# Optimization experiments

Measured on AMD Instinct MI355X. Metric: run time of the kernel, lower is better.

Reference implementation:

```python
import jax, jax.numpy as jnp
import numpy as np

B, C, N, K = 1, 64, 65536, 16

def setup_inputs() -> dict:
    key = jax.random.key(0)
    ks = jax.random.split(key, 12)
    s = 0.02
    return {
        "spa": jax.random.normal(ks[0], (B, C, N), jnp.float32),
        "spe": jax.random.normal(ks[1], (B, C, N), jnp.float32),
        "neighbor_indices": jax.random.randint(ks[2], (B, N, K), 0, N, jnp.int64),
        # spa_MHA params (torch Linear weights, shape [out,in])
        "WQ_spa": jax.random.normal(ks[3], (C, C), jnp.float32) * s,
        "WK_spa": jax.random.normal(ks[4], (C, C), jnp.float32) * s,
        "WV_spa": jax.random.normal(ks[5], (C, C), jnp.float32) * s,
        "bV_spa": jnp.zeros((C,), jnp.float32),
        # spe_MHA params
        "WQ_spe": jax.random.normal(ks[6], (C, C), jnp.float32) * s,
        "WK_spe": jax.random.normal(ks[7], (C, C), jnp.float32) * s,
        "WV_spe": jax.random.normal(ks[8], (C, C), jnp.float32) * s,
        "bV_spe": jnp.zeros((C,), jnp.float32),
    }


def _cross_att(q, nb, WQ, WK, WV, bV):
    # q: [B,N,C], nb: [B,N,K,C]
    Q = jnp.einsum('bnc,dc->bnd', q, WQ)            # [B,N,C]
    Kk = jnp.einsum('bnkc,dc->bnkd', nb, WK)        # [B,N,K,C]
    V = jnp.einsum('bnkc,dc->bnkd', nb, WV) + bV    # [B,N,K,C]
    scores = jnp.einsum('bnd,bnkd->bnk', Q, Kk) / np.sqrt(Q.shape[-1]).astype(Q.dtype)
    attn = jax.nn.softmax(scores, axis=-1)          # [B,N,K]
    ctx = jnp.einsum('bnk,bnkd->bnd', attn, V)      # [B,N,C]
    return ctx.transpose(0, 2, 1)                   # [B,C,N]


def reference(spa, spe, neighbor_indices,
              WQ_spa, WK_spa, WV_spa, bV_spa,
              WQ_spe, WK_spe, WV_spe, bV_spe):
    dims = spa.shape[1]
    feature = jnp.concatenate([spa, spe], axis=1)   # [B,2C,N]
    # gather neighbors: [B,2C,N,K]
    nb = jax.vmap(lambda f, idx: f[:, idx])(feature, neighbor_indices)
    feature_q = feature.transpose(0, 2, 1)          # [B,N,2C]
    nb = nb.transpose(0, 2, 3, 1)                   # [B,N,K,2C]
    spa_feat = _cross_att(feature_q[..., :dims], nb[..., dims:],
                          WQ_spa, WK_spa, WV_spa, bV_spa)
    spe_feat = _cross_att(feature_q[..., dims:], nb[..., :dims],
                          WQ_spe, WK_spe, WV_spe, bV_spe)
    fusion = jnp.concatenate([spa_feat, spe_feat], axis=1)  # [B,2C,N]
    return feature + fusion
```

## Files before the change

### kernel.cpp

```cpp
#include <hip/hip_runtime.h>

#define NPTS 65536

__device__ __forceinline__ float bf_lo(unsigned u) { return __uint_as_float(u << 16); }
__device__ __forceinline__ float bf_hi(unsigned u) { return __uint_as_float(u & 0xFFFF0000u); }
__device__ __forceinline__ unsigned short f2bf(float f) {
    unsigned u = __float_as_uint(f);
    return (unsigned short)((u + 0x7FFFu + ((u >> 16) & 1u)) >> 16);
}
__device__ __forceinline__ unsigned pktrunc(float a, float b) {
    return (__float_as_uint(a) >> 16) | (__float_as_uint(b) & 0xFFFF0000u);
}
__device__ __forceinline__ void unpack8(uint4 v, float* o) {
    o[0] = bf_lo(v.x); o[1] = bf_hi(v.x); o[2] = bf_lo(v.y); o[3] = bf_hi(v.y);
    o[4] = bf_lo(v.z); o[5] = bf_hi(v.z); o[6] = bf_lo(v.w); o[7] = bf_hi(v.w);
}
#if __has_builtin(__builtin_amdgcn_fdot2_f32_bf16)
typedef __bf16 bf16x2 __attribute__((ext_vector_type(2)));
__device__ __forceinline__ float dot2acc(unsigned a, unsigned b, float c) {
    return __builtin_amdgcn_fdot2_f32_bf16(__builtin_bit_cast(bf16x2, a),
                                           __builtin_bit_cast(bf16x2, b), c, false);
}
#else
__device__ __forceinline__ float dot2acc(unsigned a, unsigned b, float c) {
    return c + bf_lo(a) * bf_lo(b) + bf_hi(a) * bf_hi(b);
}
#endif
#if __has_builtin(__builtin_amdgcn_rcpf)
__device__ __forceinline__ float fastrcp(float x) { return __builtin_amdgcn_rcpf(x); }
#else
__device__ __forceinline__ float fastrcp(float x) { return 1.0f / x; }
#endif

typedef __attribute__((ext_vector_type(8))) short short8;
typedef __attribute__((ext_vector_type(4))) float f32x4;

__global__ __launch_bounds__(256) void k_matM(const float* __restrict__ WQa,
                                              const float* __restrict__ WKa,
                                              const float* __restrict__ WQe,
                                              const float* __restrict__ WKe,
                                              unsigned short* __restrict__ Mt) {
    __shared__ float WKs[4096];
    __shared__ float WQs[64][16];
    const int which = blockIdx.x >> 2;
    const int c0 = (blockIdx.x & 3) * 16;
    const float* WQ = which ? WQe : WQa;
    const float* WK = which ? WKe : WKa;
    const int t = threadIdx.x;
    #pragma unroll
    for (int i = 0; i < 16; ++i) WKs[t + i * 256] = WK[t + i * 256];
    #pragma unroll
    for (int i = 0; i < 4; ++i) {
        const int id = t + i * 256;
        WQs[id >> 4][id & 15] = WQ[(id >> 4) * 64 + c0 + (id & 15)];
    }
    __syncthreads();
    const int cc = t >> 4;
    const int eg = t & 15;
    float a0 = 0.f, a1 = 0.f, a2 = 0.f, a3 = 0.f;
    #pragma unroll
    for (int d = 0; d < 64; ++d) {
        const float wq = WQs[d][cc];
        const float4 wk = *reinterpret_cast<const float4*>(&WKs[d * 64 + eg * 4]);
        a0 += wq * wk.x; a1 += wq * wk.y; a2 += wq * wk.z; a3 += wq * wk.w;
    }
    const int c = c0 + cc;
    Mt[which * 4096 + (eg * 4 + 0) * 64 + c] = f2bf(a0);
    Mt[which * 4096 + (eg * 4 + 1) * 64 + c] = f2bf(a1);
    Mt[which * 4096 + (eg * 4 + 2) * 64 + c] = f2bf(a2);
    Mt[which * 4096 + (eg * 4 + 3) * 64 + c] = f2bf(a3);
}

__global__ __launch_bounds__(256) void k_prep(const float* __restrict__ spa,
                                              const float* __restrict__ spe,
                                              const unsigned short* __restrict__ Mt,
                                              unsigned short* __restrict__ featT,
                                              unsigned short* __restrict__ qeff) {
    __shared__ unsigned short tb[64][136];
    __shared__ unsigned short ml[2][64][72];
    const int n0 = blockIdx.x * 64;
    const int t = threadIdx.x;
    #pragma unroll
    for (int i = 0; i < 4; ++i) {
        const int id = t + i * 256;
        const int which = id >> 9;
        const int row = (id >> 3) & 63;
        const int q = id & 7;
        *reinterpret_cast<uint4*>(&ml[which][row][q * 8]) =
            *reinterpret_cast<const uint4*>(Mt + which * 4096 + row * 64 + q * 8);
    }
    {
        const int p = t & 63;
        const int c0 = t >> 6;
        #pragma unroll
        for (int i = 0; i < 32; ++i) {
            const int c = c0 + (i << 2);
            const float v = (c < 64) ? spa[c * NPTS + n0 + p]
                                     : spe[(c - 64) * NPTS + n0 + p];
            tb[p][c] = f2bf(v);
        }
    }
    __syncthreads();
    {
        const int pt = t >> 2;
        const int q = t & 3;
        const uint4* src = reinterpret_cast<const uint4*>(&tb[pt][q * 32]);
        uint4* dst = reinterpret_cast<uint4*>(featT + (size_t)(n0 + pt) * 128 + q * 32);
        dst[0] = src[0]; dst[1] = src[1]; dst[2] = src[2]; dst[3] = src[3];
    }
    const int w = t >> 6;
    const int l = t & 63;
    const int lrow = l & 15;
    const int lk8 = (l >> 4) * 8;
    short8 afr[2][2];
    #pragma unroll
    for (int half = 0; half < 2; ++half)
        #pragma unroll
        for (int kc = 0; kc < 2; ++kc)
            afr[half][kc] = __builtin_bit_cast(short8,
                *reinterpret_cast<const uint4*>(&tb[w * 16 + lrow][half * 64 + kc * 32 + lk8]));
    f32x4 acc[8];
    #pragma unroll
    for (int et = 0; et < 8; ++et) acc[et] = (f32x4){0.f, 0.f, 0.f, 0.f};
    #pragma unroll
    for (int et = 0; et < 8; ++et) {
        const int which = et >> 2;
        const int el = (et & 3) * 16 + lrow;
        #pragma unroll
        for (int kc = 0; kc < 2; ++kc) {
            const short8 bfr = __builtin_bit_cast(short8,
                *reinterpret_cast<const uint4*>(&ml[which][el][kc * 32 + lk8]));
            acc[et] = __builtin_amdgcn_mfma_f32_16x16x32_bf16(afr[which][kc], bfr, acc[et], 0, 0, 0);
        }
    }
    #pragma unroll
    for (int et = 0; et < 8; ++et) {
        #pragma unroll
        for (int r = 0; r < 4; ++r) {
            const int n = n0 + w * 16 + (l >> 4) * 4 + r;
            qeff[(size_t)n * 128 + et * 16 + lrow] = f2bf(acc[et][r]);
        }
    }
}

__global__ __launch_bounds__(256) void k_attn(const unsigned short* __restrict__ featT,
                                              const unsigned short* __restrict__ qeff,
                                              const int* __restrict__ idx,
                                              unsigned short* __restrict__ sTb) {
    __shared__ unsigned red[4][16][68];
    const int wave = threadIdx.x >> 6;
    const int lane = threadIdx.x & 63;
    const int n = blockIdx.x * 4 + wave;
    const int k = lane >> 2;
    const int c4 = lane & 3;

    const int j = idx[n * 16 + k];
    const uint4* fx = reinterpret_cast<const uint4*>(featT + (size_t)j * 128);
    const uint4 A0 = fx[2*c4],     A1 = fx[2*c4 + 1];
    const uint4 E0 = fx[8 + 2*c4], E1 = fx[8 + 2*c4 + 1];
    const uint4* qx = reinterpret_cast<const uint4*>(qeff + (size_t)n * 128);
    const uint4 QA0 = qx[2*c4],     QA1 = qx[2*c4 + 1];
    const uint4 QE0 = qx[8 + 2*c4], QE1 = qx[8 + 2*c4 + 1];

    float pa = 0.f, pe = 0.f;
    pa = dot2acc(QA0.x, E0.x, pa); pa = dot2acc(QA0.y, E0.y, pa);
    pa = dot2acc(QA0.z, E0.z, pa); pa = dot2acc(QA0.w, E0.w, pa);
    pa = dot2acc(QA1.x, E1.x, pa); pa = dot2acc(QA1.y, E1.y, pa);
    pa = dot2acc(QA1.z, E1.z, pa); pa = dot2acc(QA1.w, E1.w, pa);
    pe = dot2acc(QE0.x, A0.x, pe); pe = dot2acc(QE0.y, A0.y, pe);
    pe = dot2acc(QE0.z, A0.z, pe); pe = dot2acc(QE0.w, A0.w, pe);
    pe = dot2acc(QE1.x, A1.x, pe); pe = dot2acc(QE1.y, A1.y, pe);
    pe = dot2acc(QE1.z, A1.z, pe); pe = dot2acc(QE1.w, A1.w, pe);
    pa += __shfl_xor(pa, 1); pa += __shfl_xor(pa, 2);
    pe += __shfl_xor(pe, 1); pe += __shfl_xor(pe, 2);
    const float ea = __expf(pa * 0.125f);
    const float ee = __expf(pe * 0.125f);
    float da = ea, de = ee;
    #pragma unroll
    for (int m = 4; m < 64; m <<= 1) {
        da += __shfl_xor(da, m);
        de += __shfl_xor(de, m);
    }
    const float wA = ea * fastrcp(da);
    const float wB = ee * fastrcp(de);

    float xa[16], xe[16];
    unpack8(A0, xa); unpack8(A1, xa + 8);
    unpack8(E0, xe); unpack8(E1, xe + 8);

    unsigned pA[8], pB[8];
    #pragma unroll
    for (int i = 0; i < 8; ++i) {
        pA[i] = pktrunc(wA * xe[2*i], wA * xe[2*i + 1]);
        pB[i] = pktrunc(wB * xa[2*i], wB * xa[2*i + 1]);
    }
    {
        uint4* wa4 = reinterpret_cast<uint4*>(&red[wave][k][c4 * 8]);
        wa4[0] = make_uint4(pA[0], pA[1], pA[2], pA[3]);
        wa4[1] = make_uint4(pA[4], pA[5], pA[6], pA[7]);
        uint4* wb4 = reinterpret_cast<uint4*>(&red[wave][k][32 + c4 * 8]);
        wb4[0] = make_uint4(pB[0], pB[1], pB[2], pB[3]);
        wb4[1] = make_uint4(pB[4], pB[5], pB[6], pB[7]);
    }
    asm volatile("s_waitcnt lgkmcnt(0)" ::: "memory");
    float s0 = 0.f, s1 = 0.f;
    #pragma unroll
    for (int kk = 0; kk < 16; ++kk) {
        const unsigned v = red[wave][kk][lane];
        s0 += __uint_as_float(v << 16);
        s1 += __uint_as_float(v & 0xFFFF0000u);
    }
    reinterpret_cast<unsigned*>(sTb + (size_t)n * 128)[lane] =
        (unsigned)f2bf(s0) | ((unsigned)f2bf(s1) << 16);
}

__global__ __launch_bounds__(256, 4) void k_out(const unsigned short* __restrict__ sTb,
                                                const float* __restrict__ spa,
                                                const float* __restrict__ spe,
                                                const float* __restrict__ WVa,
                                                const float* __restrict__ bVa,
                                                const float* __restrict__ WVe,
                                                const float* __restrict__ bVe,
                                                float* __restrict__ out) {
    __shared__ char smem_raw[27136];
    unsigned short* stile = reinterpret_cast<unsigned short*>(smem_raw);
    unsigned short* wvl = reinterpret_cast<unsigned short*>(smem_raw + 8704);
    float* ctxT = reinterpret_cast<float*>(smem_raw);
    const int n0 = blockIdx.x * 32;
    const int t = threadIdx.x;
    #pragma unroll
    for (int i = 0; i < 2; ++i) {
        const int id = t + i * 256;
        const int pt = id >> 4;
        const int q = id & 15;
        *reinterpret_cast<uint4*>(stile + pt * 136 + q * 8) =
            *reinterpret_cast<const uint4*>(sTb + (size_t)(n0 + pt) * 128 + q * 8);
    }
    #pragma unroll
    for (int i = 0; i < 32; ++i) {
        const int id = t + (i << 8);
        const int which = id >> 12;
        const int d = (id >> 6) & 63;
        const int e = id & 63;
        wvl[which * 4608 + d * 72 + e] = f2bf((which ? WVe : WVa)[d * 64 + e]);
    }
    __syncthreads();
    const int w = t >> 6;
    const int l = t & 63;
    const int half = w >> 1;
    const int pg = w & 1;
    const int lrow = l & 15;
    const int lk8 = (l >> 4) * 8;
    short8 afr[2];
    #pragma unroll
    for (int kc = 0; kc < 2; ++kc)
        afr[kc] = __builtin_bit_cast(short8,
            *reinterpret_cast<const uint4*>(stile + (pg * 16 + lrow) * 136 + half * 64 + kc * 32 + lk8));
    const unsigned short* wt = wvl + half * 4608;
    const float* bV = half ? bVe : bVa;
    f32x4 acc[4];
    #pragma unroll
    for (int nt = 0; nt < 4; ++nt) {
        acc[nt] = (f32x4){0.f, 0.f, 0.f, 0.f};
        #pragma unroll
        for (int kc = 0; kc < 2; ++kc) {
            const short8 bfr = __builtin_bit_cast(short8,
                *reinterpret_cast<const uint4*>(wt + (nt * 16 + lrow) * 72 + kc * 32 + lk8));
            acc[nt] = __builtin_amdgcn_mfma_f32_16x16x32_bf16(afr[kc], bfr, acc[nt], 0, 0, 0);
        }
    }
    __syncthreads();
    #pragma unroll
    for (int nt = 0; nt < 4; ++nt) {
        const int d = nt * 16 + lrow;
        const int dglob = half * 64 + d;
        const float bias = bV[d];
        #pragma unroll
        for (int r = 0; r < 4; ++r) {
            const int pt = pg * 16 + (l >> 4) * 4 + r;
            ctxT[dglob * 33 + pt] = acc[nt][r] + bias;
        }
    }
    __syncthreads();
    {
        const int p = t & 31;
        const int ch0 = t >> 5;
        #pragma unroll
        for (int i = 0; i < 16; ++i) {
            const int ch = ch0 + (i << 3);
            const float f = (ch < 64) ? spa[ch * NPTS + n0 + p]
                                      : spe[(ch - 64) * NPTS + n0 + p];
            out[(size_t)ch * NPTS + n0 + p] = f + ctxT[ch * 33 + p];
        }
    }
}

extern "C" void kernel_launch(void* const* d_in, const int* in_sizes, int n_in,
                              void* d_out, int out_size, void* d_ws, size_t ws_size,
                              hipStream_t stream) {
    const float* spa = (const float*)d_in[0];
    const float* spe = (const float*)d_in[1];
    const int* idx   = (const int*)d_in[2];
    const float* WQa = (const float*)d_in[3];
    const float* WKa = (const float*)d_in[4];
    const float* WVa = (const float*)d_in[5];
    const float* bVa = (const float*)d_in[6];
    const float* WQe = (const float*)d_in[7];
    const float* WKe = (const float*)d_in[8];
    const float* WVe = (const float*)d_in[9];
    const float* bVe = (const float*)d_in[10];
    float* out = (float*)d_out;

    char* ws = (char*)d_ws;
    unsigned short* featT = (unsigned short*)(ws);
    unsigned short* qeff  = (unsigned short*)(ws + 16777216);
    unsigned short* sTb   = (unsigned short*)(ws + 33554432);
    unsigned short* Mt    = (unsigned short*)(ws + 50331648);

    k_matM<<<8, 256, 0, stream>>>(WQa, WKa, WQe, WKe, Mt);
    k_prep<<<1024, 256, 0, stream>>>(spa, spe, Mt, featT, qeff);
    k_attn<<<16384, 256, 0, stream>>>(featT, qeff, idx, sTb);
    k_out<<<2048, 256, 0, stream>>>(sTb, spa, spe, WVa, bVa, WVe, bVe, out);
}
```

Measured before the change: 74.99 us.

## Reuse bf16 featT for residual and precompute bf16 WV in k_matM

k_out now reads the residual from the bf16 transposed feature buffer instead of re-reading fp32 spa/spe, which halves that input traffic. The V weights are converted to bf16 once in extra k_matM blocks rather than in every k_out block. k_prep also packs two channels per shared-memory store. The cost is that the residual is added at bf16 precision rather than fp32, which adds rounding error to the output.

Result: faster. 71.63 us (-4.5%).

```diff
diff --git a/kernel.cpp b/kernel.cpp
--- a/kernel.cpp
+++ b/kernel.cpp
@@ -7,6 +7,9 @@
 __device__ __forceinline__ unsigned short f2bf(float f) {
     unsigned u = __float_as_uint(f);
     return (unsigned short)((u + 0x7FFFu + ((u >> 16) & 1u)) >> 16);
+}
+__device__ __forceinline__ float bfu(unsigned short us) {
+    return __uint_as_float(((unsigned)us) << 16);
 }
 __device__ __forceinline__ unsigned pktrunc(float a, float b) {
     return (__float_as_uint(a) >> 16) | (__float_as_uint(b) & 0xFFFF0000u);
@@ -39,14 +42,25 @@
                                               const float* __restrict__ WKa,
                                               const float* __restrict__ WQe,
                                               const float* __restrict__ WKe,
-                                              unsigned short* __restrict__ Mt) {
+                                              const float* __restrict__ WVa,
+                                              const float* __restrict__ WVe,
+                                              unsigned short* __restrict__ Mt,
+                                              unsigned short* __restrict__ WVb) {
+    const int t = threadIdx.x;
+    if (blockIdx.x >= 8) {
+        const int which = blockIdx.x - 8;
+        const float* WV = which ? WVe : WVa;
+        unsigned short* dst = WVb + which * 4096;
+        #pragma unroll
+        for (int i = 0; i < 16; ++i) dst[t + i * 256] = f2bf(WV[t + i * 256]);
+        return;
+    }
     __shared__ float WKs[4096];
     __shared__ float WQs[64][16];
     const int which = blockIdx.x >> 2;
     const int c0 = (blockIdx.x & 3) * 16;
     const float* WQ = which ? WQe : WQa;
     const float* WK = which ? WKe : WKa;
-    const int t = threadIdx.x;
     #pragma unroll
     for (int i = 0; i < 16; ++i) WKs[t + i * 256] = WK[t + i * 256];
     #pragma unroll
@@ -91,13 +105,16 @@
     }
     {
         const int p = t & 63;
-        const int c0 = t >> 6;
-        #pragma unroll
-        for (int i = 0; i < 32; ++i) {
-            const int c = c0 + (i << 2);
-            const float v = (c < 64) ? spa[c * NPTS + n0 + p]
-                                     : spe[(c - 64) * NPTS + n0 + p];
-            tb[p][c] = f2bf(v);
+        const int c0 = 2 * (t >> 6);
+        #pragma unroll
+        for (int i = 0; i < 16; ++i) {
+            const int c = c0 + 8 * i;
+            const float v0 = (c < 64) ? spa[c * NPTS + n0 + p]
+                                      : spe[(c - 64) * NPTS + n0 + p];
+            const float v1 = (c + 1 < 64) ? spa[(c + 1) * NPTS + n0 + p]
+                                          : spe[(c + 1 - 64) * NPTS + n0 + p];
+            *reinterpret_cast<unsigned*>(&tb[p][c]) =
+                (unsigned)f2bf(v0) | ((unsigned)f2bf(v1) << 16);
         }
     }
     __syncthreads();
@@ -215,11 +232,9 @@
 }
 
 __global__ __launch_bounds__(256, 4) void k_out(const unsigned short* __restrict__ sTb,
-                                                const float* __restrict__ spa,
-                                                const float* __restrict__ spe,
-                                                const float* __restrict__ WVa,
+                                                const unsigned short* __restrict__ featT,
+                                                const unsigned short* __restrict__ WVb,
                                                 const float* __restrict__ bVa,
-                                                const float* __restrict__ WVe,
                                                 const float* __restrict__ bVe,
                                                 float* __restrict__ out) {
     __shared__ char smem_raw[27136];
@@ -228,6 +243,20 @@
     float* ctxT = reinterpret_cast<float*>(smem_raw);
     const int n0 = blockIdx.x * 32;
     const int t = threadIdx.x;
+    const int w = t >> 6;
+    const int l = t & 63;
+    const int half = w >> 1;
+    const int pg = w & 1;
+    const int lrow = l & 15;
+    const int lk8 = (l >> 4) * 8;
+    unsigned short res[4][4];
+    #pragma unroll
+    for (int nt = 0; nt < 4; ++nt)
+        #pragma unroll
+        for (int r = 0; r < 4; ++r) {
+            const int pt = pg * 16 + (l >> 4) * 4 + r;
+            res[nt][r] = featT[(size_t)(n0 + pt) * 128 + half * 64 + nt * 16 + lrow];
+        }
     #pragma unroll
     for (int i = 0; i < 2; ++i) {
         const int id = t + i * 256;
@@ -237,20 +266,15 @@
             *reinterpret_cast<const uint4*>(sTb + (size_t)(n0 + pt) * 128 + q * 8);
     }
     #pragma unroll
-    for (int i = 0; i < 32; ++i) {
-        const int id = t + (i << 8);
-        const int which = id >> 12;
-        const int d = (id >> 6) & 63;
-        const int e = id & 63;
-        wvl[which * 4608 + d * 72 + e] = f2bf((which ? WVe : WVa)[d * 64 + e]);
-    }
-    __syncthreads();
-    const int w = t >> 6;
-    const int l = t & 63;
-    const int half = w >> 1;
-    const int pg = w & 1;
-    const int lrow = l & 15;
-    const int lk8 = (l >> 4) * 8;
+    for (int i = 0; i < 4; ++i) {
+        const int id = t + i * 256;
+        const int which = id >> 9;
+        const int row = (id >> 3) & 63;
+        const int q = id & 7;
+        *reinterpret_cast<uint4*>(wvl + which * 4608 + row * 72 + q * 8) =
+            *reinterpret_cast<const uint4*>(WVb + which * 4096 + row * 64 + q * 8);
+    }
+    __syncthreads();
     short8 afr[2];
     #pragma unroll
     for (int kc = 0; kc < 2; ++kc)
@@ -278,7 +302,7 @@
         #pragma unroll
         for (int r = 0; r < 4; ++r) {
             const int pt = pg * 16 + (l >> 4) * 4 + r;
-            ctxT[dglob * 33 + pt] = acc[nt][r] + bias;
+            ctxT[dglob * 33 + pt] = acc[nt][r] + bias + bfu(res[nt][r]);
         }
     }
     __syncthreads();
@@ -288,9 +312,7 @@
         #pragma unroll
         for (int i = 0; i < 16; ++i) {
             const int ch = ch0 + (i << 3);
-            const float f = (ch < 64) ? spa[ch * NPTS + n0 + p]
-                                      : spe[(ch - 64) * NPTS + n0 + p];
-            out[(size_t)ch * NPTS + n0 + p] = f + ctxT[ch * 33 + p];
+            out[(size_t)ch * NPTS + n0 + p] = ctxT[ch * 33 + p];
         }
     }
 }
@@ -316,9 +338,10 @@
     unsigned short* qeff  = (unsigned short*)(ws + 16777216);
     unsigned short* sTb   = (unsigned short*)(ws + 33554432);
     unsigned short* Mt    = (unsigned short*)(ws + 50331648);
-
-    k_matM<<<8, 256, 0, stream>>>(WQa, WKa, WQe, WKe, Mt);
+    unsigned short* WVb   = (unsigned short*)(ws + 50331648 + 16384);
+
+    k_matM<<<10, 256, 0, stream>>>(WQa, WKa, WQe, WKe, WVa, WVe, Mt, WVb);
     k_prep<<<1024, 256, 0, stream>>>(spa, spe, Mt, featT, qeff);
     k_attn<<<16384, 256, 0, stream>>>(featT, qeff, idx, sTb);
-    k_out<<<2048, 256, 0, stream>>>(sTb, spa, spe, WVa, bVa, WVe, bVe, out);
-}
+    k_out<<<2048, 256, 0, stream>>>(sTb, featT, WVb, bVa, bVe, out);
+}
```
